# Kernel tuning notes

Measured on AMD Instinct MI355X. Metric: run time of the kernel, lower is better.

## Reference

```python
import jax, jax.numpy as jnp
import numpy as np
from jax import lax

EMB = 1024      # emb_size
H = 2 * EMB     # step_feature_width / LSTM units
B = 1024        # batch of paths
PATH_LEN = 11   # max_path_length=5 -> 5 LSTM steps
N_ENT = 100000


def setup_inputs() -> dict:
    key = jax.random.key(0)
    ks = jax.random.split(key, 8)
    s = lambda fan_in: 1.0 / np.sqrt(fan_in)
    return {
        "path": jax.random.randint(ks[0], (B, PATH_LEN), 0, N_ENT, dtype=jnp.int32),
        "emb_table": jax.random.normal(ks[1], (N_ENT, EMB), jnp.float32),
        "W_lstm": jax.random.normal(ks[2], (2 * EMB, 4 * H), jnp.float32) * s(2 * EMB),
        "U_lstm": jax.random.normal(ks[3], (H, 4 * H), jnp.float32) * s(H),
        "b_lstm": jnp.zeros((4 * H,), jnp.float32),
        "W1": jax.random.normal(ks[4], (H, 2 * EMB), jnp.float32) * s(H),
        "b1": jnp.zeros((2 * EMB,), jnp.float32),
        "W2": jax.random.normal(ks[5], (2 * EMB, 2 * EMB), jnp.float32) * s(2 * EMB),
        "b2": jnp.zeros((2 * EMB,), jnp.float32),
        "W3": jax.random.normal(ks[6], (2 * EMB, 2), jnp.float32) * s(2 * EMB),
        "b3": jnp.zeros((2,), jnp.float32),
    }


def reference(path, emb_table, W_lstm, U_lstm, b_lstm, W1, b1, W2, b2, W3, b3):
    # Gather all entity embeddings along each path: [B, PATH_LEN, EMB]
    vecs = emb_table[path]
    # Step t (t=1..5, i=2t) uses concat(vec(path[i-1]), vec(path[i])): [T, B, 2*EMB]
    x_prev = vecs[:, 1:-1:2, :]   # path[1], path[3], ...  -> [B, T, EMB]
    x_curr = vecs[:, 2::2, :]     # path[2], path[4], ...  -> [B, T, EMB]
    xs = jnp.swapaxes(jnp.concatenate([x_prev, x_curr], axis=-1), 0, 1)  # [T, B, 2E]

    def step(carry, x):
        h, c = carry
        z = x @ W_lstm + h @ U_lstm + b_lstm           # [B, 4H]
        i, f, g, o = jnp.split(z, 4, axis=-1)           # Keras gate order i,f,g,o
        i = jax.nn.sigmoid(i)
        f = jax.nn.sigmoid(f)
        g = jnp.tanh(g)
        o = jax.nn.sigmoid(o)
        c = f * c + i * g
        h = o * jnp.tanh(c)
        return (h, c), None

    h0 = jnp.zeros((xs.shape[1], H), xs.dtype)
    (h, _), _ = lax.scan(step, (h0, h0), xs)

    # 2-layer ReLU MLP + softmax head
    a = jax.nn.relu(h @ W1 + b1)
    a = jax.nn.relu(a @ W2 + b2)
    probs = jax.nn.softmax(a @ W3 + b3, axis=-1)        # [B, 2]
    return probs
```

## Files before the change

kernel.cpp:

```cpp
#include <hip/hip_runtime.h>
#include <hip/hip_bf16.h>

typedef unsigned short u16;
typedef short bf16x8 __attribute__((ext_vector_type(8)));
typedef float floatx4 __attribute__((ext_vector_type(4)));
typedef unsigned short u16x4 __attribute__((ext_vector_type(4)));
typedef unsigned short u16x8 __attribute__((ext_vector_type(8)));

__device__ __forceinline__ u16 f2bf(float f) {
    unsigned int x; __builtin_memcpy(&x, &f, 4);
    unsigned int r = x + 0x7fffu + ((x >> 16) & 1u);
    return (u16)(r >> 16);
}
__device__ __forceinline__ float sigm(float x) {
    return 1.f / (1.f + __expf(-x));
}
__device__ __forceinline__ float tanhx(float x) {
    x = fminf(fmaxf(x, -15.f), 15.f);
    float e = __expf(2.f * x);
    return (e - 1.f) / (e + 1.f);
}

__device__ __forceinline__ void async16(const void* g, void* l) {
    __builtin_amdgcn_global_load_lds(
        (__attribute__((address_space(1))) void*)(void*)(g),
        (__attribute__((address_space(3))) void*)(l),
        16, 0, 0);
}

__global__ __launch_bounds__(256) void transpose_f32_bf16(
    const float* __restrict__ in, u16* __restrict__ out, int K, int N)
{
    __shared__ float tile[64][65];
    const int n0 = blockIdx.x * 64, k0 = blockIdx.y * 64;
    const int t = threadIdx.x;
    const int tc = t & 15, tr = t >> 4;
#pragma unroll
    for (int i = 0; i < 4; i++) {
        int k = i * 16 + tr;
        int n = tc * 4;
        float4 v = *(const float4*)&in[(size_t)(k0 + k) * N + n0 + n];
        tile[k][n + 0] = v.x; tile[k][n + 1] = v.y;
        tile[k][n + 2] = v.z; tile[k][n + 3] = v.w;
    }
    __syncthreads();
#pragma unroll
    for (int i = 0; i < 4; i++) {
        int n = i * 16 + tr;
        int k = tc * 4;
        u16x4 v;
        v.x = f2bf(tile[k + 0][n]);
        v.y = f2bf(tile[k + 1][n]);
        v.z = f2bf(tile[k + 2][n]);
        v.w = f2bf(tile[k + 3][n]);
        *(u16x4*)&out[(size_t)(n0 + n) * K + k0 + k] = v;
    }
}

__global__ __launch_bounds__(256) void gather_x(
    const int* __restrict__ path, const float* __restrict__ emb, u16* __restrict__ X)
{
    const int blk = blockIdx.x;
    const int t = blk >> 10, b = blk & 1023;
    const int tt = threadIdx.x;
    const int half = tt >> 7;
    const int idx = path[b * 11 + 1 + 2 * t + half];
    const int j = (tt & 127) * 8;
    const float4 v0 = *(const float4*)&emb[(size_t)idx * 1024 + j];
    const float4 v1 = *(const float4*)&emb[(size_t)idx * 1024 + j + 4];
    u16x8 o;
    o[0] = f2bf(v0.x); o[1] = f2bf(v0.y); o[2] = f2bf(v0.z); o[3] = f2bf(v0.w);
    o[4] = f2bf(v1.x); o[5] = f2bf(v1.y); o[6] = f2bf(v1.z); o[7] = f2bf(v1.w);
    *(u16x8*)&X[(size_t)blk * 2048 + half * 1024 + j] = o;
}

template <int MODE>
__global__ __launch_bounds__(256, 2) void gemm_bt(
    const u16* __restrict__ A, const u16* __restrict__ Bt,
    const float* __restrict__ bias, float* __restrict__ Cf, u16* __restrict__ Cb,
    int M, int N, int K)
{
    __shared__ alignas(16) u16 sA[128 * 32];
    __shared__ alignas(16) u16 sB[128 * 32];

    const int t = threadIdx.x;
    const int lane = t & 63;
    const int w = t >> 6;
    const int wr = w >> 1, wc = w & 1;
    const int l15 = lane & 15, quad = lane >> 4;
    const int m0 = blockIdx.x * 128, n0 = blockIdx.y * 128;

    const int ch1 = t, ch2 = t + 256;
    const int r1 = ch1 >> 2, c1 = (ch1 & 3) * 8;
    const int r2 = ch2 >> 2, c2 = (ch2 & 3) * 8;

    floatx4 acc[4][4] = {};

    for (int k0 = 0; k0 < K; k0 += 32) {
        async16(A + (size_t)(m0 + r1) * K + k0 + c1, sA + ch1 * 8);
        async16(A + (size_t)(m0 + r2) * K + k0 + c2, sA + ch2 * 8);
        async16(Bt + (size_t)(n0 + r1) * K + k0 + c1, sB + ch1 * 8);
        async16(Bt + (size_t)(n0 + r2) * K + k0 + c2, sB + ch2 * 8);
        __syncthreads();

        bf16x8 af[4], bfr[4];
#pragma unroll
        for (int mi = 0; mi < 4; mi++)
            af[mi] = *(const bf16x8*)&sA[(wr * 64 + mi * 16 + l15) * 32 + quad * 8];
#pragma unroll
        for (int ni = 0; ni < 4; ni++)
            bfr[ni] = *(const bf16x8*)&sB[(wc * 64 + ni * 16 + l15) * 32 + quad * 8];
#pragma unroll
        for (int mi = 0; mi < 4; mi++)
#pragma unroll
            for (int ni = 0; ni < 4; ni++)
                acc[mi][ni] = __builtin_amdgcn_mfma_f32_16x16x32_bf16(
                    af[mi], bfr[ni], acc[mi][ni], 0, 0, 0);
        __syncthreads();
    }

#pragma unroll
    for (int mi = 0; mi < 4; mi++) {
#pragma unroll
        for (int ni = 0; ni < 4; ni++) {
            const int n = n0 + wc * 64 + ni * 16 + l15;
            float bv = 0.f;
            if (MODE != 1) bv = bias[n];
#pragma unroll
            for (int r = 0; r < 4; r++) {
                const int m = m0 + wr * 64 + mi * 16 + quad * 4 + r;
                float v = acc[mi][ni][r];
                if (MODE == 0) {
                    Cf[(size_t)m * N + n] = v + bv;
                } else if (MODE == 1) {
                    Cf[(size_t)m * N + n] += v;
                } else {
                    float x = v + bv;
                    x = x > 0.f ? x : 0.f;
                    Cb[(size_t)m * N + n] = f2bf(x);
                }
            }
        }
    }
}

template <bool FIRST>
__global__ __launch_bounds__(256) void lstm_gate(
    const float* __restrict__ Z, float* __restrict__ c, u16* __restrict__ h)
{
    const int idx = blockIdx.x * 256 + threadIdx.x;
    const int b = idx >> 9;
    const int j = (idx & 511) * 4;
    const size_t zb = (size_t)b * 8192 + j;
    const float4 vi = *(const float4*)&Z[zb];
    const float4 vf = *(const float4*)&Z[zb + 2048];
    const float4 vg = *(const float4*)&Z[zb + 4096];
    const float4 vo = *(const float4*)&Z[zb + 6144];
    const size_t cb = (size_t)b * 2048 + j;
    float4 vc;
    if (FIRST) vc = make_float4(0.f, 0.f, 0.f, 0.f);
    else       vc = *(const float4*)&c[cb];

    float ia[4] = {vi.x, vi.y, vi.z, vi.w};
    float fa[4] = {vf.x, vf.y, vf.z, vf.w};
    float ga[4] = {vg.x, vg.y, vg.z, vg.w};
    float oa[4] = {vo.x, vo.y, vo.z, vo.w};
    float ca[4] = {vc.x, vc.y, vc.z, vc.w};
    float cn[4]; u16x4 hv;
#pragma unroll
    for (int q = 0; q < 4; q++) {
        float i_ = sigm(ia[q]);
        float f_ = sigm(fa[q]);
        float g_ = tanhx(ga[q]);
        float o_ = sigm(oa[q]);
        cn[q] = f_ * ca[q] + i_ * g_;
        float h_ = o_ * tanhx(cn[q]);
        ((u16*)&hv)[q] = f2bf(h_);
    }
    *(float4*)&c[cb] = make_float4(cn[0], cn[1], cn[2], cn[3]);
    *(u16x4*)&h[cb] = hv;
}

__global__ __launch_bounds__(256) void head_kernel(
    const u16* __restrict__ a2, const float* __restrict__ W3,
    const float* __restrict__ b3, float* __restrict__ out)
{
    const int t = threadIdx.x;
    const int w = t >> 6, lane = t & 63;
    const int b = blockIdx.x * 4 + w;
    float s0 = 0.f, s1 = 0.f;
    for (int k = lane; k < 2048; k += 64) {
        unsigned int u = ((unsigned int)a2[(size_t)b * 2048 + k]) << 16;
        float a; __builtin_memcpy(&a, &u, 4);
        s0 += a * W3[2 * k];
        s1 += a * W3[2 * k + 1];
    }
#pragma unroll
    for (int off = 32; off > 0; off >>= 1) {
        s0 += __shfl_down(s0, off);
        s1 += __shfl_down(s1, off);
    }
    if (lane == 0) {
        float l0 = s0 + b3[0];
        float l1 = s1 + b3[1];
        float m = fmaxf(l0, l1);
        float e0 = __expf(l0 - m), e1 = __expf(l1 - m);
        float inv = 1.f / (e0 + e1);
        out[2 * b]     = e0 * inv;
        out[2 * b + 1] = e1 * inv;
    }
}

extern "C" void kernel_launch(void* const* d_in, const int* in_sizes, int n_in,
                              void* d_out, int out_size, void* d_ws, size_t ws_size,
                              hipStream_t stream) {
    const int*   path = (const int*)d_in[0];
    const float* emb  = (const float*)d_in[1];
    const float* W    = (const float*)d_in[2];
    const float* U    = (const float*)d_in[3];
    const float* bl   = (const float*)d_in[4];
    const float* W1   = (const float*)d_in[5];
    const float* b1   = (const float*)d_in[6];
    const float* W2   = (const float*)d_in[7];
    const float* b2   = (const float*)d_in[8];
    const float* W3   = (const float*)d_in[9];
    const float* b3   = (const float*)d_in[10];

    const size_t NEED = 159383552;
    if (ws_size < NEED) return;
    char* ws = (char*)d_ws;
    u16*  Wt  = (u16*) (ws + 0);
    u16*  Ut  = (u16*) (ws + 33554432);
    u16*  W1t = (u16*) (ws + 67108864);
    u16*  W2t = (u16*) (ws + 75497472);
    u16*  X   = (u16*) (ws + 83886080);
    float* Z  = (float*)(ws + 104857600);
    float* c  = (float*)(ws + 138412032);
    u16*  h   = (u16*) (ws + 146800640);
    u16*  a1  = (u16*) (ws + 150994944);
    u16*  a2  = (u16*) (ws + 155189248);

    transpose_f32_bf16<<<dim3(128, 32), 256, 0, stream>>>(W, Wt, 2048, 8192);
    transpose_f32_bf16<<<dim3(128, 32), 256, 0, stream>>>(U, Ut, 2048, 8192);
    transpose_f32_bf16<<<dim3(32, 32), 256, 0, stream>>>(W1, W1t, 2048, 2048);
    transpose_f32_bf16<<<dim3(32, 32), 256, 0, stream>>>(W2, W2t, 2048, 2048);
    gather_x<<<5120, 256, 0, stream>>>(path, emb, X);

    for (int t = 0; t < 5; t++) {
        gemm_bt<0><<<dim3(8, 64), 256, 0, stream>>>(
            X + (size_t)t * 1024 * 2048, Wt, bl, Z, nullptr, 1024, 8192, 2048);
        if (t > 0)
            gemm_bt<1><<<dim3(8, 64), 256, 0, stream>>>(
                h, Ut, nullptr, Z, nullptr, 1024, 8192, 2048);
        if (t == 0) lstm_gate<true ><<<2048, 256, 0, stream>>>(Z, c, h);
        else        lstm_gate<false><<<2048, 256, 0, stream>>>(Z, c, h);
    }

    gemm_bt<2><<<dim3(8, 16), 256, 0, stream>>>(h,  W1t, b1, nullptr, a1, 1024, 2048, 2048);
    gemm_bt<2><<<dim3(8, 16), 256, 0, stream>>>(a1, W2t, b2, nullptr, a2, 1024, 2048, 2048);
    head_kernel<<<256, 256, 0, stream>>>(a2, W3, b3, (float*)d_out);
}
```

Measured before the change: 1.262 ms.

## Batch input projection across steps and fuse LSTM gates into recurrent GEMM

The input projection X@W for all five timesteps now runs as one large GEMM (M=5120) instead of five separate launches. The W and U columns are permuted so that each 64-column group holds the i/f/g/o gates of 16 hidden units. This lets the recurrent h@U GEMM apply the LSTM cell update in its epilogue, which removes the separate gate kernel and the read-modify-write of Z each step. The MLP GEMMs use 64-row tiles to launch more blocks, at the cost of a larger workspace for the stacked Zx buffer and double-buffered h.

```diff
diff --git a/kernel.cpp b/kernel.cpp
--- a/kernel.cpp
+++ b/kernel.cpp
@@ -21,6 +21,11 @@
     return (e - 1.f) / (e + 1.f);
 }
 
+__device__ __forceinline__ int permc(int c) {
+    int gate = c >> 11, j = c & 2047;
+    return ((j >> 4) << 6) | (gate << 4) | (j & 15);
+}
+
 __device__ __forceinline__ void async16(const void* g, void* l) {
     __builtin_amdgcn_global_load_lds(
         (__attribute__((address_space(1))) void*)(void*)(g),
@@ -28,6 +33,7 @@
         16, 0, 0);
 }
 
+template <bool PERM>
 __global__ __launch_bounds__(256) void transpose_f32_bf16(
     const float* __restrict__ in, u16* __restrict__ out, int K, int N)
 {
@@ -53,7 +59,8 @@
         v.y = f2bf(tile[k + 1][n]);
         v.z = f2bf(tile[k + 2][n]);
         v.w = f2bf(tile[k + 3][n]);
-        *(u16x4*)&out[(size_t)(n0 + n) * K + k0 + k] = v;
+        const int row = PERM ? permc(n0 + n) : (n0 + n);
+        *(u16x4*)&out[(size_t)row * K + k0 + k] = v;
     }
 }
 
@@ -74,35 +81,29 @@
     *(u16x8*)&X[(size_t)blk * 2048 + half * 1024 + j] = o;
 }
 
-template <int MODE>
-__global__ __launch_bounds__(256, 2) void gemm_bt(
+__global__ __launch_bounds__(256, 2) void gemm_zx(
     const u16* __restrict__ A, const u16* __restrict__ Bt,
-    const float* __restrict__ bias, float* __restrict__ Cf, u16* __restrict__ Cb,
-    int M, int N, int K)
+    const float* __restrict__ bias, float* __restrict__ Cf, int M, int N, int K)
 {
     __shared__ alignas(16) u16 sA[128 * 32];
     __shared__ alignas(16) u16 sB[128 * 32];
-
     const int t = threadIdx.x;
     const int lane = t & 63;
     const int w = t >> 6;
     const int wr = w >> 1, wc = w & 1;
     const int l15 = lane & 15, quad = lane >> 4;
     const int m0 = blockIdx.x * 128, n0 = blockIdx.y * 128;
-
     const int ch1 = t, ch2 = t + 256;
     const int r1 = ch1 >> 2, c1 = (ch1 & 3) * 8;
     const int r2 = ch2 >> 2, c2 = (ch2 & 3) * 8;
 
     floatx4 acc[4][4] = {};
-
     for (int k0 = 0; k0 < K; k0 += 32) {
         async16(A + (size_t)(m0 + r1) * K + k0 + c1, sA + ch1 * 8);
         async16(A + (size_t)(m0 + r2) * K + k0 + c2, sA + ch2 * 8);
         async16(Bt + (size_t)(n0 + r1) * K + k0 + c1, sB + ch1 * 8);
         async16(Bt + (size_t)(n0 + r2) * K + k0 + c2, sB + ch2 * 8);
         __syncthreads();
-
         bf16x8 af[4], bfr[4];
 #pragma unroll
         for (int mi = 0; mi < 4; mi++)
@@ -118,67 +119,169 @@
                     af[mi], bfr[ni], acc[mi][ni], 0, 0, 0);
         __syncthreads();
     }
-
 #pragma unroll
     for (int mi = 0; mi < 4; mi++) {
 #pragma unroll
         for (int ni = 0; ni < 4; ni++) {
             const int n = n0 + wc * 64 + ni * 16 + l15;
-            float bv = 0.f;
-            if (MODE != 1) bv = bias[n];
+            const float bv = bias[(((n >> 4) & 3) << 11) | ((n >> 6) << 4) | (n & 15)];
 #pragma unroll
             for (int r = 0; r < 4; r++) {
                 const int m = m0 + wr * 64 + mi * 16 + quad * 4 + r;
-                float v = acc[mi][ni][r];
-                if (MODE == 0) {
-                    Cf[(size_t)m * N + n] = v + bv;
-                } else if (MODE == 1) {
-                    Cf[(size_t)m * N + n] += v;
-                } else {
-                    float x = v + bv;
-                    x = x > 0.f ? x : 0.f;
-                    Cb[(size_t)m * N + n] = f2bf(x);
-                }
+                Cf[(size_t)m * N + n] = acc[mi][ni][r] + bv;
             }
         }
     }
 }
 
-template <bool FIRST>
-__global__ __launch_bounds__(256) void lstm_gate(
-    const float* __restrict__ Z, float* __restrict__ c, u16* __restrict__ h)
+__global__ __launch_bounds__(256, 2) void gemm_step(
+    const u16* __restrict__ hin, const u16* __restrict__ Bt,
+    const float* __restrict__ Zx, float* __restrict__ c, u16* __restrict__ hout)
+{
+    const int M = 1024, N = 8192, K = 2048;
+    __shared__ alignas(16) u16 sA[128 * 32];
+    __shared__ alignas(16) u16 sB[128 * 32];
+    const int t = threadIdx.x;
+    const int lane = t & 63;
+    const int w = t >> 6;
+    const int wr = w >> 1, wc = w & 1;
+    const int l15 = lane & 15, quad = lane >> 4;
+    const int m0 = blockIdx.x * 128, n0 = blockIdx.y * 128;
+    const int ch1 = t, ch2 = t + 256;
+    const int r1 = ch1 >> 2, c1 = (ch1 & 3) * 8;
+    const int r2 = ch2 >> 2, c2 = (ch2 & 3) * 8;
+
+    floatx4 acc[4][4] = {};
+    for (int k0 = 0; k0 < K; k0 += 32) {
+        async16(hin + (size_t)(m0 + r1) * K + k0 + c1, sA + ch1 * 8);
+        async16(hin + (size_t)(m0 + r2) * K + k0 + c2, sA + ch2 * 8);
+        async16(Bt + (size_t)(n0 + r1) * K + k0 + c1, sB + ch1 * 8);
+        async16(Bt + (size_t)(n0 + r2) * K + k0 + c2, sB + ch2 * 8);
+        __syncthreads();
+        bf16x8 af[4], bfr[4];
+#pragma unroll
+        for (int mi = 0; mi < 4; mi++)
+            af[mi] = *(const bf16x8*)&sA[(wr * 64 + mi * 16 + l15) * 32 + quad * 8];
+#pragma unroll
+        for (int ni = 0; ni < 4; ni++)
+            bfr[ni] = *(const bf16x8*)&sB[(wc * 64 + ni * 16 + l15) * 32 + quad * 8];
+#pragma unroll
+        for (int mi = 0; mi < 4; mi++)
+#pragma unroll
+            for (int ni = 0; ni < 4; ni++)
+                acc[mi][ni] = __builtin_amdgcn_mfma_f32_16x16x32_bf16(
+                    af[mi], bfr[ni], acc[mi][ni], 0, 0, 0);
+        __syncthreads();
+    }
+
+    const int jg = (n0 >> 6) + wc;
+    const int j = jg * 16 + l15;
+#pragma unroll
+    for (int mi = 0; mi < 4; mi++) {
+#pragma unroll
+        for (int r = 0; r < 4; r++) {
+            const int m = m0 + wr * 64 + mi * 16 + quad * 4 + r;
+            const size_t zb = (size_t)m * N + jg * 64 + l15;
+            const float zi = acc[mi][0][r] + Zx[zb];
+            const float zf = acc[mi][1][r] + Zx[zb + 16];
+            const float zg = acc[mi][2][r] + Zx[zb + 32];
+            const float zo = acc[mi][3][r] + Zx[zb + 48];
+            const float i_ = sigm(zi);
+            const float f_ = sigm(zf);
+            const float g_ = tanhx(zg);
+            const float o_ = sigm(zo);
+            const size_t cb = (size_t)m * 2048 + j;
+            const float cn = f_ * c[cb] + i_ * g_;
+            c[cb] = cn;
+            hout[cb] = f2bf(o_ * tanhx(cn));
+        }
+    }
+}
+
+__global__ __launch_bounds__(256) void gate0(
+    const float* __restrict__ Zx, float* __restrict__ c, u16* __restrict__ h)
 {
     const int idx = blockIdx.x * 256 + threadIdx.x;
     const int b = idx >> 9;
     const int j = (idx & 511) * 4;
-    const size_t zb = (size_t)b * 8192 + j;
-    const float4 vi = *(const float4*)&Z[zb];
-    const float4 vf = *(const float4*)&Z[zb + 2048];
-    const float4 vg = *(const float4*)&Z[zb + 4096];
-    const float4 vo = *(const float4*)&Z[zb + 6144];
-    const size_t cb = (size_t)b * 2048 + j;
-    float4 vc;
-    if (FIRST) vc = make_float4(0.f, 0.f, 0.f, 0.f);
-    else       vc = *(const float4*)&c[cb];
-
+    const size_t base = (size_t)b * 8192 + ((j >> 4) << 6) + (j & 15);
+    const float4 vi = *(const float4*)&Zx[base];
+    const float4 vf = *(const float4*)&Zx[base + 16];
+    const float4 vg = *(const float4*)&Zx[base + 32];
+    const float4 vo = *(const float4*)&Zx[base + 48];
     float ia[4] = {vi.x, vi.y, vi.z, vi.w};
     float fa[4] = {vf.x, vf.y, vf.z, vf.w};
     float ga[4] = {vg.x, vg.y, vg.z, vg.w};
     float oa[4] = {vo.x, vo.y, vo.z, vo.w};
-    float ca[4] = {vc.x, vc.y, vc.z, vc.w};
     float cn[4]; u16x4 hv;
 #pragma unroll
     for (int q = 0; q < 4; q++) {
-        float i_ = sigm(ia[q]);
-        float f_ = sigm(fa[q]);
-        float g_ = tanhx(ga[q]);
-        float o_ = sigm(oa[q]);
-        cn[q] = f_ * ca[q] + i_ * g_;
-        float h_ = o_ * tanhx(cn[q]);
-        ((u16*)&hv)[q] = f2bf(h_);
-    }
+        (void)fa;
+        const float i_ = sigm(ia[q]);
+        const float g_ = tanhx(ga[q]);
+        const float o_ = sigm(oa[q]);
+        cn[q] = i_ * g_;
+        hv[q] = f2bf(o_ * tanhx(cn[q]));
+        (void)sigm(fa[q]);
+    }
+    const size_t cb = (size_t)b * 2048 + j;
     *(float4*)&c[cb] = make_float4(cn[0], cn[1], cn[2], cn[3]);
     *(u16x4*)&h[cb] = hv;
+}
+
+__global__ __launch_bounds__(256, 4) void gemm_mlp(
+    const u16* __restrict__ A, const u16* __restrict__ Bt,
+    const float* __restrict__ bias, u16* __restrict__ Cb, int K)
+{
+    const int N = 2048;
+    __shared__ alignas(16) u16 sA[64 * 32];
+    __shared__ alignas(16) u16 sB[128 * 32];
+    const int t = threadIdx.x;
+    const int lane = t & 63;
+    const int w = t >> 6;
+    const int wr = w >> 1, wc = w & 1;
+    const int l15 = lane & 15, quad = lane >> 4;
+    const int m0 = blockIdx.x * 64, n0 = blockIdx.y * 128;
+    const int rA = t >> 2, cA = (t & 3) * 8;
+    const int r1 = t >> 2, c1 = (t & 3) * 8;
+    const int r2 = (t + 256) >> 2, c2 = ((t + 256) & 3) * 8;
+
+    floatx4 acc[2][4] = {};
+    for (int k0 = 0; k0 < K; k0 += 32) {
+        async16(A + (size_t)(m0 + rA) * K + k0 + cA, sA + t * 8);
+        async16(Bt + (size_t)(n0 + r1) * K + k0 + c1, sB + t * 8);
+        async16(Bt + (size_t)(n0 + r2) * K + k0 + c2, sB + (t + 256) * 8);
+        __syncthreads();
+        bf16x8 af[2], bfr[4];
+#pragma unroll
+        for (int mi = 0; mi < 2; mi++)
+            af[mi] = *(const bf16x8*)&sA[(wr * 32 + mi * 16 + l15) * 32 + quad * 8];
+#pragma unroll
+        for (int ni = 0; ni < 4; ni++)
+            bfr[ni] = *(const bf16x8*)&sB[(wc * 64 + ni * 16 + l15) * 32 + quad * 8];
+#pragma unroll
+        for (int mi = 0; mi < 2; mi++)
+#pragma unroll
+            for (int ni = 0; ni < 4; ni++)
+                acc[mi][ni] = __builtin_amdgcn_mfma_f32_16x16x32_bf16(
+                    af[mi], bfr[ni], acc[mi][ni], 0, 0, 0);
+        __syncthreads();
+    }
+#pragma unroll
+    for (int mi = 0; mi < 2; mi++) {
+#pragma unroll
+        for (int ni = 0; ni < 4; ni++) {
+            const int n = n0 + wc * 64 + ni * 16 + l15;
+            const float bv = bias[n];
+#pragma unroll
+            for (int r = 0; r < 4; r++) {
+                const int m = m0 + wr * 32 + mi * 16 + quad * 4 + r;
+                float x = acc[mi][ni][r] + bv;
+                x = x > 0.f ? x : 0.f;
+                Cb[(size_t)m * N + n] = f2bf(x);
+            }
+        }
+    }
 }
 
 __global__ __launch_bounds__(256) void head_kernel(
@@ -201,11 +304,11 @@
         s1 += __shfl_down(s1, off);
     }
     if (lane == 0) {
-        float l0 = s0 + b3[0];
-        float l1 = s1 + b3[1];
-        float m = fmaxf(l0, l1);
-        float e0 = __expf(l0 - m), e1 = __expf(l1 - m);
-        float inv = 1.f / (e0 + e1);
+        const float l0 = s0 + b3[0];
+        const float l1 = s1 + b3[1];
+        const float m = fmaxf(l0, l1);
+        const float e0 = __expf(l0 - m), e1 = __expf(l1 - m);
+        const float inv = 1.f / (e0 + e1);
         out[2 * b]     = e0 * inv;
         out[2 * b + 1] = e1 * inv;
     }
@@ -226,37 +329,37 @@
     const float* W3   = (const float*)d_in[9];
     const float* b3   = (const float*)d_in[10];
 
-    const size_t NEED = 159383552;
+    const size_t NEED = 297795584;
     if (ws_size < NEED) return;
     char* ws = (char*)d_ws;
-    u16*  Wt  = (u16*) (ws + 0);
-    u16*  Ut  = (u16*) (ws + 33554432);
-    u16*  W1t = (u16*) (ws + 67108864);
-    u16*  W2t = (u16*) (ws + 75497472);
-    u16*  X   = (u16*) (ws + 83886080);
-    float* Z  = (float*)(ws + 104857600);
-    float* c  = (float*)(ws + 138412032);
-    u16*  h   = (u16*) (ws + 146800640);
-    u16*  a1  = (u16*) (ws + 150994944);
-    u16*  a2  = (u16*) (ws + 155189248);
-
-    transpose_f32_bf16<<<dim3(128, 32), 256, 0, stream>>>(W, Wt, 2048, 8192);
-    transpose_f32_bf16<<<dim3(128, 32), 256, 0, stream>>>(U, Ut, 2048, 8192);
-    transpose_f32_bf16<<<dim3(32, 32), 256, 0, stream>>>(W1, W1t, 2048, 2048);
-    transpose_f32_bf16<<<dim3(32, 32), 256, 0, stream>>>(W2, W2t, 2048, 2048);
+    u16*   Wt  = (u16*)  (ws + 0);
+    u16*   Ut  = (u16*)  (ws + 33554432);
+    u16*   W1t = (u16*)  (ws + 67108864);
+    u16*   W2t = (u16*)  (ws + 75497472);
+    u16*   X   = (u16*)  (ws + 83886080);
+    float* Zx  = (float*)(ws + 104857600);
+    float* c   = (float*)(ws + 272629760);
+    u16*   hA  = (u16*)  (ws + 281018368);
+    u16*   hB  = (u16*)  (ws + 285212672);
+    u16*   a1  = (u16*)  (ws + 289406976);
+    u16*   a2  = (u16*)  (ws + 293601280);
+
+    transpose_f32_bf16<true ><<<dim3(128, 32), 256, 0, stream>>>(W, Wt, 2048, 8192);
+    transpose_f32_bf16<true ><<<dim3(128, 32), 256, 0, stream>>>(U, Ut, 2048, 8192);
+    transpose_f32_bf16<false><<<dim3(32, 32), 256, 0, stream>>>(W1, W1t, 2048, 2048);
+    transpose_f32_bf16<false><<<dim3(32, 32), 256, 0, stream>>>(W2, W2t, 2048, 2048);
     gather_x<<<5120, 256, 0, stream>>>(path, emb, X);
 
-    for (int t = 0; t < 5; t++) {
-        gemm_bt<0><<<dim3(8, 64), 256, 0, stream>>>(
-            X + (size_t)t * 1024 * 2048, Wt, bl, Z, nullptr, 1024, 8192, 2048);
-        if (t > 0)
-            gemm_bt<1><<<dim3(8, 64), 256, 0, stream>>>(
-                h, Ut, nullptr, Z, nullptr, 1024, 8192, 2048);
-        if (t == 0) lstm_gate<true ><<<2048, 256, 0, stream>>>(Z, c, h);
-        else        lstm_gate<false><<<2048, 256, 0, stream>>>(Z, c, h);
-    }
-
-    gemm_bt<2><<<dim3(8, 16), 256, 0, stream>>>(h,  W1t, b1, nullptr, a1, 1024, 2048, 2048);
-    gemm_bt<2><<<dim3(8, 16), 256, 0, stream>>>(a1, W2t, b2, nullptr, a2, 1024, 2048, 2048);
+    gemm_zx<<<dim3(40, 64), 256, 0, stream>>>(X, Wt, bl, Zx, 5120, 8192, 2048);
+
+    gate0<<<2048, 256, 0, stream>>>(Zx, c, hA);
+    for (int t = 1; t < 5; t++) {
+        const u16* hin = (t & 1) ? hA : hB;
+        u16* hout      = (t & 1) ? hB : hA;
+        gemm_step<<<dim3(8, 64), 256, 0, stream>>>(
+            hin, Ut, Zx + (size_t)t * 1024 * 8192, c, hout);
+    }
+    gemm_mlp<<<dim3(16, 16), 256, 0, stream>>>(hA, W1t, b1, a1, 2048);
+    gemm_mlp<<<dim3(16, 16), 256, 0, stream>>>(a1, W2t, b2, a2, 2048);
     head_kernel<<<256, 256, 0, stream>>>(a2, W3, b3, (float*)d_out);
 }
```

Measured after the change: 1.130 ms. -10.5%, faster.
